# Kernel tuning notes

Measured on AMD Instinct MI355X. Metric: run time of the kernel, lower is better.

The kernel has to match this reference:

```python
import jax, jax.numpy as jnp
import numpy as np

# ---- static config (matches init_kwargs) ----
B, CIN, H, W = 32, 64, 32, 32
CO, K, G, PAD = 64, 7, 8, 3
R_RAMP = 3.0            # ramp size R
Z_INIT = 4.0            # initial adaptive-span value
MAXSZ = W // 2          # adaptive_mask max_size = image_size/2 = 16
CPG = CO // G           # channels per group


def _unfold(t, k):
    # torch x.unfold(2,k,1).unfold(3,k,1): [B,C,Hp,Wp] -> [B,C,Ho,Wo,kh,kw]
    ho = t.shape[2] - k + 1
    wo = t.shape[3] - k + 1
    return jnp.stack(
        [jnp.stack([t[:, :, i:i + ho, j:j + wo] for j in range(k)], axis=-1)
         for i in range(k)], axis=-2)


def _adaptive_mask(current_val):
    # AdaptiveMask.forward applied to [B,G,CPG,H,W]; x.shape[-1] == W.
    # one_d_mask[g, i] is the soft value written on 'ring' i (rows i and W-1-i,
    # columns spanning the ring interval) of a WxW mask.
    template = jnp.linspace(1.0 - MAXSZ, 0.0, MAXSZ)            # [MAXSZ]
    om = (template[None, :] + current_val * MAXSZ) / R_RAMP + 1.0
    om = jnp.clip(om, 0.0, 1.0)                                  # [G, MAXSZ]
    # (slice [-(W//2):] is identity since MAXSZ == W//2)
    i = jnp.arange(W)
    r = jnp.minimum(i, W - 1 - i)                                # ring index per row
    top = i <= (W - 1 - i)
    lo = jnp.where(top, r, r + 1)    # bottom row of ring misses its leftmost col
    hi = W - 1 - r
    c = jnp.arange(W)
    in_ring = (c[None, :] >= lo[:, None]) & (c[None, :] <= hi[:, None])  # [W,W]
    vals = om[:, r]                                              # [G, W]
    return jnp.where(in_ring[None, :, :], vals[:, :, None], 1.0)  # [G,W,W]


def setup_inputs() -> dict:
    key = jax.random.key(0)
    ks = jax.random.split(key, 6)
    x = jax.random.normal(ks[0], (B, CIN, H, W), dtype=jnp.float32)
    fan_out_std = np.sqrt(2.0 / CO).astype(np.float32)  # kaiming fan_out, 1x1 conv
    w_q = jax.random.normal(ks[1], (CO, CIN), dtype=jnp.float32) * fan_out_std
    w_k = jax.random.normal(ks[2], (CO, CIN), dtype=jnp.float32) * fan_out_std
    w_v = jax.random.normal(ks[3], (CO, CIN), dtype=jnp.float32) * fan_out_std
    rel_h = jax.random.normal(ks[4], (CO // 2, 1, 1, K, 1), dtype=jnp.float32)
    rel_w = jax.random.normal(ks[5], (CO // 2, 1, 1, 1, K), dtype=jnp.float32)
    current_val = jnp.full((G, 1), Z_INIT, dtype=jnp.float32)
    return {"x": x, "w_q": w_q, "w_k": w_k, "w_v": w_v,
            "rel_h": rel_h, "rel_w": rel_w, "current_val": current_val}


def reference(x, w_q, w_k, w_v, rel_h, rel_w, current_val):
    q = jnp.einsum('bchw,oc->bohw', x, w_q)                       # [B,CO,H,W]
    xp = jnp.pad(x, ((0, 0), (0, 0), (PAD, PAD), (PAD, PAD)))
    k = jnp.einsum('bchw,oc->bohw', xp, w_k)
    v = jnp.einsum('bchw,oc->bohw', xp, w_v)
    k = _unfold(k, K)                                             # [B,CO,H,W,K,K]
    v = _unfold(v, K)
    k_h, k_w = jnp.split(k, 2, axis=1)
    k = jnp.concatenate([k_h + rel_h, k_w + rel_w], axis=1)
    k = k.reshape(B, G, CPG, H, W, K * K)
    v = v.reshape(B, G, CPG, H, W, K * K)
    q = q.reshape(B, G, CPG, H, W, 1)
    scores = jnp.sum(q * k, axis=2)                               # [B,G,H,W,K*K]
    attn = jax.nn.softmax(scores, axis=-1)
    out = jnp.sum(attn[:, :, None] * v, axis=-1)                  # [B,G,CPG,H,W]
    mask = _adaptive_mask(current_val)                            # [G,W,W]
    return out * mask[None, :, None, :, :]
```

## Files before the change

### kernel.cpp

```cpp
#include <hip/hip_runtime.h>

#define BB    32
#define CINc  64
#define HHc   32
#define WWc   32
#define COc   64
#define KSc   7
#define GGc   8
#define PADc  3
#define CPGc  8
#define NPIX  (HHc * WWc)
#define HROWS 19
#define NPOSH (HROWS * 32)
#define NPOSP 640

typedef _Float16 h8    __attribute__((ext_vector_type(8)));
typedef _Float16 h2    __attribute__((ext_vector_type(2)));
typedef float    f32x4 __attribute__((ext_vector_type(4)));

#if defined(__has_builtin)
#if __has_builtin(__builtin_amdgcn_fdot2)
#define HAVE_FDOT2 1
#endif
#endif

__global__ __launch_bounds__(512, 4) void fused_kernel(
    const float* __restrict__ x,
    const float* __restrict__ wq,
    const float* __restrict__ wk,
    const float* __restrict__ wv,
    const float* __restrict__ rel_h,
    const float* __restrict__ rel_w,
    const float* __restrict__ cv,
    float* __restrict__ out)
{
    __shared__ __attribute__((aligned(16))) f32x4 kplv[NPOSP];
    __shared__ __attribute__((aligned(16))) f32x4 vplv[NPOSP];
    __shared__ __attribute__((aligned(16))) f32x4 qplv[NPOSP];

    const int bi   = blockIdx.x;
    const int xcd  = bi & 7;
    const int t0   = bi >> 3;
    const int im   = t0 & 3;
    const int rest = t0 >> 2;
    const int g    = rest >> 1;
    const int hf   = rest & 1;
    const int b    = im * 8 + xcd;
    const int o0   = g * CPGc;
    const int tid  = threadIdx.x;

    const int rowbase = hf ? (HHc - HROWS) : 0;
    const int pgbase  = rowbase * WWc;

    const int lane = tid & 63;
    const int wid  = tid >> 6;
    const int an   = lane & 15;
    const int quad = lane >> 4;

    const float* xb = x + (size_t)b * CINc * NPIX;

    h8 bf[2][2];
    {
        const float* br0 = (an < 8) ? (wk + (o0 + an) * CINc)
                                    : (wv + (o0 + an - 8) * CINc);
        const float* br1 = wq + (o0 + ((an < 8) ? an : 0)) * CINc;
#pragma unroll
        for (int ks = 0; ks < 2; ++ks) {
            const int c0 = ks * 32 + quad * 8;
#pragma unroll
            for (int jj = 0; jj < 8; ++jj) {
                bf[0][ks][jj] = (_Float16)br0[c0 + jj];
                bf[1][ks][jj] = (_Float16)br1[c0 + jj];
            }
        }
    }

    _Float16* kp16 = (_Float16*)kplv;
    _Float16* qp16 = (_Float16*)qplv;
    _Float16* vp16 = (_Float16*)vplv;

#pragma unroll 1
    for (int tt = wid; tt < 10; tt += 8) {
        const int pbase = pgbase + tt * 64;

        f32x4 acc0[4], acc1[4];
#pragma unroll
        for (int m = 0; m < 4; ++m) { acc0[m] = (f32x4)0.f; acc1[m] = (f32x4)0.f; }

#pragma unroll
        for (int m = 0; m < 4; ++m) {
            const int pg = min(pbase + m * 16 + an, NPIX - 1);
            const float* xpx = xb + pg;
#pragma unroll
            for (int ks = 0; ks < 2; ++ks) {
                const int c0 = ks * 32 + quad * 8;
                h8 a;
#pragma unroll
                for (int jj = 0; jj < 8; ++jj)
                    a[jj] = (_Float16)xpx[(c0 + jj) * NPIX];
                acc0[m] = __builtin_amdgcn_mfma_f32_16x16x32_f16(a, bf[0][ks], acc0[m], 0, 0, 0);
                acc1[m] = __builtin_amdgcn_mfma_f32_16x16x32_f16(a, bf[1][ks], acc1[m], 0, 0, 0);
            }
        }

#pragma unroll
        for (int m = 0; m < 4; ++m) {
#pragma unroll
            for (int r = 0; r < 4; ++r) {
                const int lp = tt * 64 + m * 16 + quad * 4 + r;
                const float d0 = acc0[m][r];
                if (an < 8) {
                    kp16[lp * 8 + an] = (_Float16)d0;
                    qp16[lp * 8 + an] = (_Float16)acc1[m][r];
                } else {
                    vp16[lp * 8 + (an - 8)] = (_Float16)d0;
                }
            }
        }
    }

    __syncthreads();

    const int w  = tid & 31;
    const int lh = tid >> 5;
    const int h  = hf * 16 + lh;

    f32x4 qraw = qplv[(h - rowbase) * WWc + w];
    const h2* qh = (const h2*)&qraw;
    h2 q2[4] = {qh[0], qh[1], qh[2], qh[3]};
    float qf[CPGc];
#pragma unroll
    for (int jj = 0; jj < 4; ++jj) {
        qf[2 * jj]     = (float)q2[jj].x;
        qf[2 * jj + 1] = (float)q2[jj].y;
    }

    const bool use_h = (g < 4);
    const float* relp = use_h ? (rel_h + o0 * KSc) : (rel_w + (o0 - 32) * KSc);
    float qrel[KSc];
#pragma unroll
    for (int tt = 0; tt < KSc; ++tt) {
        float s = 0.f;
#pragma unroll
        for (int oi = 0; oi < CPGc; ++oi)
            s = fmaf(qf[oi], relp[oi * KSc + tt], s);
        qrel[tt] = s;
    }

    int  xcl[KSc];
    bool xin[KSc];
#pragma unroll
    for (int kj = 0; kj < KSc; ++kj) {
        const int xx = w + kj - PADc;
        xin[kj] = (xx >= 0) && (xx < WWc);
        xcl[kj] = min(max(xx, 0), WWc - 1);
    }

    float den = 0.f;
    float acc[CPGc];
#pragma unroll
    for (int oi = 0; oi < CPGc; ++oi) acc[oi] = 0.f;

#pragma unroll
    for (int ki = 0; ki < KSc; ++ki) {
        const int y    = h + ki - PADc;
        const bool yin = (y >= 0) && (y < HHc);
        const int base = (min(max(y, 0), HHc - 1) - rowbase) * WWc;
#pragma unroll
        for (int kj = 0; kj < KSc; ++kj) {
            const int p = base + xcl[kj];
            const f32x4 kraw = kplv[p];
            const f32x4 vraw = vplv[p];
            const bool in = yin && xin[kj];

            float d = 0.f;
            const h2* kh = (const h2*)&kraw;
            const h2* vh = (const h2*)&vraw;
#if HAVE_FDOT2
            d = __builtin_amdgcn_fdot2(q2[0], kh[0], d, false);
            d = __builtin_amdgcn_fdot2(q2[1], kh[1], d, false);
            d = __builtin_amdgcn_fdot2(q2[2], kh[2], d, false);
            d = __builtin_amdgcn_fdot2(q2[3], kh[3], d, false);
#else
#pragma unroll
            for (int jj = 0; jj < 4; ++jj) {
                d = fmaf(qf[2 * jj],     (float)kh[jj].x, d);
                d = fmaf(qf[2 * jj + 1], (float)kh[jj].y, d);
            }
#endif
            const float s = (use_h ? qrel[ki] : qrel[kj]) + (in ? d : 0.f);
            const float e = __expf(s);
            den += e;
            const float ev = in ? e : 0.f;
            acc[0] = fmaf(ev, (float)vh[0].x, acc[0]);
            acc[1] = fmaf(ev, (float)vh[0].y, acc[1]);
            acc[2] = fmaf(ev, (float)vh[1].x, acc[2]);
            acc[3] = fmaf(ev, (float)vh[1].y, acc[3]);
            acc[4] = fmaf(ev, (float)vh[2].x, acc[4]);
            acc[5] = fmaf(ev, (float)vh[2].y, acc[5]);
            acc[6] = fmaf(ev, (float)vh[3].x, acc[6]);
            acc[7] = fmaf(ev, (float)vh[3].y, acc[7]);
        }
    }

    const int  r  = min(h, HHc - 1 - h);
    const int  lo = (h <= HHc - 1 - h) ? r : r + 1;
    const int  hi = HHc - 1 - r;
    const bool in_ring = (w >= lo) && (w <= hi);
    const float cvg = cv[g];
    float om = ((float)r - 15.0f + cvg * 16.0f) * (1.0f / 3.0f) + 1.0f;
    om = fminf(fmaxf(om, 0.0f), 1.0f);
    const float maskv = in_ring ? om : 1.0f;
    const float scale = maskv / den;

    float* ob = out + ((size_t)b * COc + o0) * NPIX + h * WWc + w;
#pragma unroll
    for (int oi = 0; oi < CPGc; ++oi)
        ob[(size_t)oi * NPIX] = acc[oi] * scale;
}

extern "C" void kernel_launch(void* const* d_in, const int* in_sizes, int n_in,
                              void* d_out, int out_size, void* d_ws, size_t ws_size,
                              hipStream_t stream) {
    const float* x     = (const float*)d_in[0];
    const float* wq    = (const float*)d_in[1];
    const float* wk    = (const float*)d_in[2];
    const float* wv    = (const float*)d_in[3];
    const float* rel_h = (const float*)d_in[4];
    const float* rel_w = (const float*)d_in[5];
    const float* cv    = (const float*)d_in[6];
    float* out = (float*)d_out;

    fused_kernel<<<512, 512, 0, stream>>>(x, wq, wk, wv, rel_h, rel_w, cv, out);
}
```

Measured before the change: 87.69 us.

## Split 7x7 attention taps across two thread halves with shared-memory reduction

New measurement: 129.7 us. +47.9%, slower.

```diff
diff --git a/kernel.cpp b/kernel.cpp
--- a/kernel.cpp
+++ b/kernel.cpp
@@ -11,7 +11,6 @@
 #define CPGc  8
 #define NPIX  (HHc * WWc)
 #define HROWS 19
-#define NPOSH (HROWS * 32)
 #define NPOSP 640
 
 typedef _Float16 h8    __attribute__((ext_vector_type(8)));
@@ -24,7 +23,7 @@
 #endif
 #endif
 
-__global__ __launch_bounds__(512, 4) void fused_kernel(
+__global__ __launch_bounds__(1024, 8) void fused_kernel(
     const float* __restrict__ x,
     const float* __restrict__ wq,
     const float* __restrict__ wk,
@@ -37,6 +36,9 @@
     __shared__ __attribute__((aligned(16))) f32x4 kplv[NPOSP];
     __shared__ __attribute__((aligned(16))) f32x4 vplv[NPOSP];
     __shared__ __attribute__((aligned(16))) f32x4 qplv[NPOSP];
+    __shared__ __attribute__((aligned(16))) f32x4 exacc0[512];
+    __shared__ __attribute__((aligned(16))) f32x4 exacc1[512];
+    __shared__ float exden[512];
 
     const int bi   = blockIdx.x;
     const int xcd  = bi & 7;
@@ -75,55 +77,59 @@
         }
     }
 
-    _Float16* kp16 = (_Float16*)kplv;
-    _Float16* qp16 = (_Float16*)qplv;
-    _Float16* vp16 = (_Float16*)vplv;
+    {
+        _Float16* kp16 = (_Float16*)kplv;
+        _Float16* qp16 = (_Float16*)qplv;
+        _Float16* vp16 = (_Float16*)vplv;
 
 #pragma unroll 1
-    for (int tt = wid; tt < 10; tt += 8) {
-        const int pbase = pgbase + tt * 64;
-
-        f32x4 acc0[4], acc1[4];
-#pragma unroll
-        for (int m = 0; m < 4; ++m) { acc0[m] = (f32x4)0.f; acc1[m] = (f32x4)0.f; }
-
-#pragma unroll
-        for (int m = 0; m < 4; ++m) {
-            const int pg = min(pbase + m * 16 + an, NPIX - 1);
-            const float* xpx = xb + pg;
-#pragma unroll
-            for (int ks = 0; ks < 2; ++ks) {
-                const int c0 = ks * 32 + quad * 8;
-                h8 a;
-#pragma unroll
-                for (int jj = 0; jj < 8; ++jj)
-                    a[jj] = (_Float16)xpx[(c0 + jj) * NPIX];
-                acc0[m] = __builtin_amdgcn_mfma_f32_16x16x32_f16(a, bf[0][ks], acc0[m], 0, 0, 0);
-                acc1[m] = __builtin_amdgcn_mfma_f32_16x16x32_f16(a, bf[1][ks], acc1[m], 0, 0, 0);
+        for (int tt = wid; tt < 10; tt += 16) {
+            const int pbase = pgbase + tt * 64;
+
+            f32x4 acc0[4], acc1[4];
+#pragma unroll
+            for (int m = 0; m < 4; ++m) { acc0[m] = (f32x4)0.f; acc1[m] = (f32x4)0.f; }
+
+#pragma unroll
+            for (int m = 0; m < 4; ++m) {
+                const int pg = min(pbase + m * 16 + an, NPIX - 1);
+                const float* xpx = xb + pg;
+#pragma unroll
+                for (int ks = 0; ks < 2; ++ks) {
+                    const int c0 = ks * 32 + quad * 8;
+                    h8 a;
+#pragma unroll
+                    for (int jj = 0; jj < 8; ++jj)
+                        a[jj] = (_Float16)xpx[(c0 + jj) * NPIX];
+                    acc0[m] = __builtin_amdgcn_mfma_f32_16x16x32_f16(a, bf[0][ks], acc0[m], 0, 0, 0);
+                    acc1[m] = __builtin_amdgcn_mfma_f32_16x16x32_f16(a, bf[1][ks], acc1[m], 0, 0, 0);
+                }
+            }
+
+#pragma unroll
+            for (int m = 0; m < 4; ++m) {
+#pragma unroll
+                for (int r = 0; r < 4; ++r) {
+                    const int lp = tt * 64 + m * 16 + quad * 4 + r;
+                    const float d0 = acc0[m][r];
+                    if (an < 8) {
+                        kp16[lp * 8 + an] = (_Float16)d0;
+                        qp16[lp * 8 + an] = (_Float16)acc1[m][r];
+                    } else {
+                        vp16[lp * 8 + (an - 8)] = (_Float16)d0;
+                    }
+                }
             }
         }
-
-#pragma unroll
-        for (int m = 0; m < 4; ++m) {
-#pragma unroll
-            for (int r = 0; r < 4; ++r) {
-                const int lp = tt * 64 + m * 16 + quad * 4 + r;
-                const float d0 = acc0[m][r];
-                if (an < 8) {
-                    kp16[lp * 8 + an] = (_Float16)d0;
-                    qp16[lp * 8 + an] = (_Float16)acc1[m][r];
-                } else {
-                    vp16[lp * 8 + (an - 8)] = (_Float16)d0;
-                }
-            }
-        }
     }
 
     __syncthreads();
 
-    const int w  = tid & 31;
-    const int lh = tid >> 5;
-    const int h  = hf * 16 + lh;
+    const int sub = tid >> 9;
+    const int px  = tid & 511;
+    const int w   = px & 31;
+    const int lh  = px >> 5;
+    const int h   = hf * 16 + lh;
 
     f32x4 qraw = qplv[(h - rowbase) * WWc + w];
     const h2* qh = (const h2*)&qraw;
@@ -161,8 +167,7 @@
 #pragma unroll
     for (int oi = 0; oi < CPGc; ++oi) acc[oi] = 0.f;
 
-#pragma unroll
-    for (int ki = 0; ki < KSc; ++ki) {
+    auto tap_row = [&](int ki) {
         const int y    = h + ki - PADc;
         const bool yin = (y >= 0) && (y < HHc);
         const int base = (min(max(y, 0), HHc - 1) - rowbase) * WWc;
@@ -201,22 +206,43 @@
             acc[6] = fmaf(ev, (float)vh[3].x, acc[6]);
             acc[7] = fmaf(ev, (float)vh[3].y, acc[7]);
         }
-    }
-
-    const int  r  = min(h, HHc - 1 - h);
-    const int  lo = (h <= HHc - 1 - h) ? r : r + 1;
-    const int  hi = HHc - 1 - r;
-    const bool in_ring = (w >= lo) && (w <= hi);
-    const float cvg = cv[g];
-    float om = ((float)r - 15.0f + cvg * 16.0f) * (1.0f / 3.0f) + 1.0f;
-    om = fminf(fmaxf(om, 0.0f), 1.0f);
-    const float maskv = in_ring ? om : 1.0f;
-    const float scale = maskv / den;
-
-    float* ob = out + ((size_t)b * COc + o0) * NPIX + h * WWc + w;
-#pragma unroll
-    for (int oi = 0; oi < CPGc; ++oi)
-        ob[(size_t)oi * NPIX] = acc[oi] * scale;
+    };
+
+    if (sub == 0) {
+#pragma unroll
+        for (int ki = 0; ki < 4; ++ki) tap_row(ki);
+    } else {
+#pragma unroll
+        for (int ki = 4; ki < KSc; ++ki) tap_row(ki);
+        exden[px]  = den;
+        exacc0[px] = (f32x4){acc[0], acc[1], acc[2], acc[3]};
+        exacc1[px] = (f32x4){acc[4], acc[5], acc[6], acc[7]};
+    }
+
+    __syncthreads();
+
+    if (sub == 0) {
+        den += exden[px];
+        const f32x4 a0 = exacc0[px];
+        const f32x4 a1 = exacc1[px];
+        acc[0] += a0.x; acc[1] += a0.y; acc[2] += a0.z; acc[3] += a0.w;
+        acc[4] += a1.x; acc[5] += a1.y; acc[6] += a1.z; acc[7] += a1.w;
+
+        const int  r  = min(h, HHc - 1 - h);
+        const int  lo = (h <= HHc - 1 - h) ? r : r + 1;
+        const int  hi = HHc - 1 - r;
+        const bool in_ring = (w >= lo) && (w <= hi);
+        const float cvg = cv[g];
+        float om = ((float)r - 15.0f + cvg * 16.0f) * (1.0f / 3.0f) + 1.0f;
+        om = fminf(fmaxf(om, 0.0f), 1.0f);
+        const float maskv = in_ring ? om : 1.0f;
+        const float scale = maskv / den;
+
+        float* ob = out + ((size_t)b * COc + o0) * NPIX + h * WWc + w;
+#pragma unroll
+        for (int oi = 0; oi < CPGc; ++oi)
+            ob[(size_t)oi * NPIX] = acc[oi] * scale;
+    }
 }
 
 extern "C" void kernel_launch(void* const* d_in, const int* in_sizes, int n_in,
@@ -231,5 +257,5 @@
     const float* cv    = (const float*)d_in[6];
     float* out = (float*)d_out;
 
-    fused_kernel<<<512, 512, 0, stream>>>(x, wq, wk, wv, rel_h, rel_w, cv, out);
+    fused_kernel<<<512, 1024, 0, stream>>>(x, wq, wk, wv, rel_h, rel_w, cv, out);
 }
```
